# Performance work log

Hardware: AMD Instinct MI355X
Metric: run time of the kernel (lower is better)

Reference implementation:

```python
import jax, jax.numpy as jnp
import numpy as np

B, S, K, N, G = 4, 2048, 4096, 11008, 128  # batch, seq, in_features, out_features, groupsize


def setup_inputs() -> dict:
    key = jax.random.key(0)
    k1, k2, k3, k4 = jax.random.split(key, 4)
    x = jax.random.normal(k1, (B, S, K), dtype=jnp.float32)
    # unpacked int4 codes in [0, 16)
    weight_q = jax.random.randint(k2, (N, K), 0, 16, dtype=jnp.int32)
    # groupwise scales (positive, small) and zeros, packed as [K//G, N, 2]
    scales = jax.random.uniform(k3, (K // G, N), dtype=jnp.float32) * 0.02 + 1e-3
    zeros = jax.random.normal(k4, (K // G, N), dtype=jnp.float32) * 0.1
    scales_and_zeros = jnp.stack([scales, zeros], axis=-1)  # [K//G, N, 2]
    return {"x": x, "weight_q": weight_q, "scales_and_zeros": scales_and_zeros}


def reference(x, weight_q, scales_and_zeros):
    # Dequantize groupwise: w[n,k] = (q[n,k] - 8) * scale[k//G, n] + zero[k//G, n]
    scales = scales_and_zeros[..., 0].T  # [N, K//G]
    zeros = scales_and_zeros[..., 1].T   # [N, K//G]
    q = weight_q.astype(x.dtype).reshape(N, K // G, G)  # [N, K//G, G]
    w = (q - 8.0) * scales[:, :, None] + zeros[:, :, None]  # fused dequant
    w = w.reshape(N, K)
    # y[b,s,n] = sum_k x[b,s,k] * w[n,k]
    return jnp.einsum("bsk,nk->bsn", x, w)
```

## Files before the change

kernel.cpp:

```cpp
#include <hip/hip_runtime.h>
#include <stdint.h>


typedef __attribute__((ext_vector_type(8))) short short8;
typedef __attribute__((ext_vector_type(4))) float float4v;
typedef __attribute__((ext_vector_type(4))) int int4v;
typedef __attribute__((ext_vector_type(2))) float float2v;
typedef __attribute__((ext_vector_type(4))) unsigned short ushort4v;

static constexpr int M_ = 8192;
static constexpr int K_ = 4096;
static constexpr int N_ = 11008;
static constexpr int NKT = K_ / 64;

__device__ __forceinline__ unsigned short f2bf(float f) {
    union { float f; uint32_t u; } v;
    v.f = f;
    uint32_t u = v.u;
    u += 0x7fffu + ((u >> 16) & 1u);
    return (unsigned short)(u >> 16);
}

__device__ __forceinline__ void gload16(const void* g, void* l) {
    __builtin_amdgcn_global_load_lds(
        (const __attribute__((address_space(1))) uint32_t*)g,
        (__attribute__((address_space(3))) uint32_t*)l, 16, 0, 0);
}

__global__ __launch_bounds__(256) void cvt_x_kernel(const float* __restrict__ X,
                                                    unsigned short* __restrict__ Xb) {
    const int i = blockIdx.x * 256 + threadIdx.x;
    const float4v a = ((const float4v*)X)[2 * (size_t)i];
    const float4v b = ((const float4v*)X)[2 * (size_t)i + 1];
    short8 o;
    #pragma unroll
    for (int j = 0; j < 4; ++j) o[j] = (short)f2bf(a[j]);
    #pragma unroll
    for (int j = 0; j < 4; ++j) o[4 + j] = (short)f2bf(b[j]);
    ((short8*)Xb)[(size_t)i] = o;
}

__global__ __launch_bounds__(256) void deq_w_kernel(const int* __restrict__ Q,
                                                    const float* __restrict__ SZ,
                                                    unsigned short* __restrict__ Wb) {
    const int i = blockIdx.x * 256 + threadIdx.x;
    const int n = i >> 9;
    const int c = i & 511;
    const int k0 = c * 8;
    const int g = k0 >> 7;
    const float2v sz = *(const float2v*)(SZ + ((size_t)g * N_ + n) * 2);
    const float s = sz[0], z = sz[1];
    const int4v q0 = *(const int4v*)(Q + (size_t)n * K_ + k0);
    const int4v q1 = *(const int4v*)(Q + (size_t)n * K_ + k0 + 4);
    short8 o;
    #pragma unroll
    for (int j = 0; j < 4; ++j) o[j] = (short)f2bf((float)(q0[j] - 8) * s + z);
    #pragma unroll
    for (int j = 0; j < 4; ++j) o[4 + j] = (short)f2bf((float)(q1[j] - 8) * s + z);
    ((short8*)Wb)[(size_t)i] = o;
}


template <int BUF, int MH>
__device__ __forceinline__ void read_a(const char* ldsB, short8 (&a)[4][2],
                                       int aK0, int aK1) {
    constexpr int base = BUF * 32768 + MH * 16384;
    #pragma unroll
    for (int i = 0; i < 4; ++i) {
        a[i][0] = *(const short8*)(ldsB + base + i * 2048 + aK0);
        a[i][1] = *(const short8*)(ldsB + base + i * 2048 + aK1);
    }
}

template <int BUF, int NH>
__device__ __forceinline__ void read_b(const char* ldsB, short8 (&b)[2][2],
                                       int bK0, int bK1) {
    constexpr int base = BUF * 32768 + NH * 16384;
    #pragma unroll
    for (int j = 0; j < 2; ++j) {
        b[j][0] = *(const short8*)(ldsB + base + j * 2048 + bK0);
        b[j][1] = *(const short8*)(ldsB + base + j * 2048 + bK1);
    }
}

template <int MH, int NH>
__device__ __forceinline__ void phase_mma(short8 (&a)[4][2], short8 (&b)[2][2],
                                          float4v (&acc)[8][4]) {
    __builtin_amdgcn_s_setprio(1);
    #pragma unroll
    for (int i = 0; i < 4; ++i)
        #pragma unroll
        for (int j = 0; j < 2; ++j) {
            acc[MH * 4 + i][NH * 2 + j] = __builtin_amdgcn_mfma_f32_16x16x32_bf16(
                a[i][0], b[j][0], acc[MH * 4 + i][NH * 2 + j], 0, 0, 0);
            acc[MH * 4 + i][NH * 2 + j] = __builtin_amdgcn_mfma_f32_16x16x32_bf16(
                a[i][1], b[j][1], acc[MH * 4 + i][NH * 2 + j], 0, 0, 0);
        }
    __builtin_amdgcn_s_setprio(0);
}

#define SBAR() __builtin_amdgcn_sched_barrier(0)
#define VMW(n) asm volatile("s_waitcnt vmcnt(" #n ")" ::: "memory")
#define LGKM(n) asm volatile("s_waitcnt lgkmcnt(" #n ")" ::: "memory")
#define BARRIER() __builtin_amdgcn_s_barrier()

__global__ __launch_bounds__(512, 2) void gemm_bf16_8ph(
    const unsigned short* __restrict__ Agl,
    const unsigned short* __restrict__ Bgl,
    float* __restrict__ C) {
    __shared__ alignas(16) unsigned short lds[65536];

    const int tid = threadIdx.x;
    const int lane = tid & 63;
    const int wid = tid >> 6;
    const int wr = wid >> 2;
    const int wc = wid & 3;

    const int bid = blockIdx.x;
    const int wg = (bid & 7) * 172 + (bid >> 3);
    const int mt = wg / 43;
    const int nt = wg % 43;
    const int row0 = mt * 256;
    const int col0 = nt * 256;

    const int r8 = lane >> 3;
    const int kc = ((lane & 7) ^ r8) * 8;

    const int l15 = lane & 15;
    const int k0o = ((lane >> 4) * 16) ^ ((l15 & 7) << 4);
    const int k1o = k0o ^ 64;
    const int aK0 = (wr * 64 + l15) * 128 + k0o;
    const int aK1 = (wr * 64 + l15) * 128 + k1o;
    const int bK0 = 65536 + (wc * 32 + l15) * 128 + k0o;
    const int bK1 = 65536 + (wc * 32 + l15) * 128 + k1o;
    const char* ldsB = (const char*)lds;
    unsigned short* ldsU = lds;
    const char* AglB = (const char*)Agl;
    const char* BglB = (const char*)Bgl;

    uint32_t sA[2][2], sB[2][2];
    #pragma unroll
    for (int h = 0; h < 2; ++h)
        #pragma unroll
        for (int i = 0; i < 2; ++i) {
            sA[h][i] = (uint32_t)(row0 + h * 128 + (wid * 2 + i) * 8 + r8) * (K_ * 2)
                       + (uint32_t)kc * 2;
            sB[h][i] = (uint32_t)(col0 + h * 128 + (wid * 2 + i) * 8 + r8) * (K_ * 2)
                       + (uint32_t)kc * 2;
        }

    auto gA = [&](uint32_t& off, int b, int h, int i) {
        gload16(AglB + off, ldsU + b * 16384 + (h * 128 + (wid * 2 + i) * 8) * 64);
        off += 128;
    };
    auto gB = [&](uint32_t& off, int b, int h, int i) {
        gload16(BglB + off, ldsU + 32768 + b * 16384 + (h * 128 + (wid * 2 + i) * 8) * 64);
        off += 128;
    };

    float4v acc[8][4] = {};

    gA(sA[0][0], 0, 0, 0); gA(sA[0][1], 0, 0, 1);
    gB(sB[0][0], 0, 0, 0); gB(sB[0][1], 0, 0, 1);
    gB(sB[1][0], 0, 1, 0); gB(sB[1][1], 0, 1, 1);
    gA(sA[1][0], 0, 1, 0); gA(sA[1][1], 0, 1, 1);
    VMW(4);
    BARRIER(); SBAR();

#define KTILE(BUF, DN, W1, W2, W3, DOEND)                                   \
    {                                                                       \
        short8 a0[4][2], a1[4][2], b0[2][2], b1[2][2];                      \
                                   \
        read_a<BUF, 0>(ldsB, a0, aK0, aK1);                                 \
        read_b<BUF, 0>(ldsB, b0, bK0, bK1);                                 \
        if (DN) { gA(sA[0][0], (BUF) ^ 1, 0, 0); gA(sA[0][1], (BUF) ^ 1, 0, 1); } \
        LGKM(8);                                                            \
        BARRIER(); SBAR();                                                  \
        LGKM(0); SBAR();                                                    \
        phase_mma<0, 0>(a0, b0, acc);                                       \
        VMW(W1);                                                            \
        BARRIER(); SBAR();                                                  \
                                       \
        read_b<BUF, 1>(ldsB, b1, bK0, bK1);                                 \
        if (DN) { gB(sB[0][0], (BUF) ^ 1, 0, 0); gB(sB[0][1], (BUF) ^ 1, 0, 1); } \
        BARRIER(); SBAR();                                                  \
        LGKM(0); SBAR();                                                    \
        phase_mma<0, 1>(a0, b1, acc);                                       \
        VMW(W2);                                                            \
        BARRIER(); SBAR();                                                  \
                                       \
        read_a<BUF, 1>(ldsB, a1, aK0, aK1);                                 \
        if (DN) { gB(sB[1][0], (BUF) ^ 1, 1, 0); gB(sB[1][1], (BUF) ^ 1, 1, 1); } \
        BARRIER(); SBAR();                                                  \
        LGKM(0); SBAR();                                                    \
        phase_mma<1, 0>(a1, b0, acc);                                       \
        BARRIER(); SBAR();                                                  \
                                          \
        if (DN) { gA(sA[1][0], (BUF) ^ 1, 1, 0); gA(sA[1][1], (BUF) ^ 1, 1, 1); } \
        phase_mma<1, 1>(a1, b1, acc);                                       \
        if (DOEND) {                                                        \
            VMW(W3);                                                        \
            BARRIER(); SBAR();                                              \
        }                                                                   \
    }

    for (int t2 = 0; t2 < NKT - 2; t2 += 2) {
        KTILE(0, 1, 4, 4, 4, 1);
        KTILE(1, 1, 4, 4, 4, 1);
    }
    KTILE(0, 1, 4, 4, 4, 1);
    KTILE(1, 0, 2, 0, 0, 0);
#undef KTILE

    const int lrow = (lane >> 4) * 4;
    #pragma unroll
    for (int mf = 0; mf < 8; ++mf)
        #pragma unroll
        for (int nf = 0; nf < 4; ++nf)
            #pragma unroll
            for (int j = 0; j < 4; ++j) {
                const int r = row0 + (mf >> 2) * 128 + wr * 64 + (mf & 3) * 16 + lrow + j;
                const int c = col0 + (nf >> 1) * 128 + wc * 32 + (nf & 1) * 16 + l15;
                C[(size_t)r * N_ + c] = acc[mf][nf][j];
            }
}

static constexpr int LDSS = 40;

__global__ __launch_bounds__(256, 2) void w4_gemm_fused(
    const float* __restrict__ X, const int* __restrict__ Q,
    const float* __restrict__ SZ, float* __restrict__ C) {
    __shared__ alignas(16) unsigned short As[128 * LDSS];
    __shared__ alignas(16) unsigned short Ws[128 * LDSS];
    const int tid = threadIdx.x;
    const int lane = tid & 63;
    const int wid = tid >> 6;
    const int wrr = wid >> 1;
    const int wcc = wid & 1;
    const int row0 = blockIdx.x * 128;
    const int col0 = blockIdx.y * 128;
    float4v acc[4][4] = {};
    float4v a_reg[4];
    int4v q_reg[4];
    float2v sz_reg[4];

    auto load_tile = [&](int kb) {
        const int g = kb >> 7;
        #pragma unroll
        for (int i = 0; i < 4; ++i) {
            const int idx = tid + 256 * i;
            const int r = idx >> 3;
            const int v = idx & 7;
            a_reg[i] = *(const float4v*)(X + (size_t)(row0 + r) * K_ + kb + v * 4);
            q_reg[i] = *(const int4v*)(Q + (size_t)(col0 + r) * K_ + kb + v * 4);
            sz_reg[i] = *(const float2v*)(SZ + ((size_t)g * N_ + (col0 + r)) * 2);
        }
    };
    auto write_tile = [&]() {
        #pragma unroll
        for (int i = 0; i < 4; ++i) {
            const int idx = tid + 256 * i;
            const int r = idx >> 3;
            const int v = idx & 7;
            ushort4v ab, wb;
            #pragma unroll
            for (int j = 0; j < 4; ++j) ab[j] = f2bf(a_reg[i][j]);
            const float s = sz_reg[i][0];
            const float z = sz_reg[i][1];
            #pragma unroll
            for (int j = 0; j < 4; ++j) wb[j] = f2bf((float)(q_reg[i][j] - 8) * s + z);
            *(ushort4v*)(&As[r * LDSS + v * 4]) = ab;
            *(ushort4v*)(&Ws[r * LDSS + v * 4]) = wb;
        }
    };
    auto compute = [&]() {
        const int lr = lane & 15;
        const int lg = lane >> 4;
        short8 af[4], bf[4];
        #pragma unroll
        for (int mf = 0; mf < 4; ++mf)
            af[mf] = *(const short8*)(&As[(wrr * 64 + mf * 16 + lr) * LDSS + lg * 8]);
        #pragma unroll
        for (int nf = 0; nf < 4; ++nf)
            bf[nf] = *(const short8*)(&Ws[(wcc * 64 + nf * 16 + lr) * LDSS + lg * 8]);
        #pragma unroll
        for (int mf = 0; mf < 4; ++mf)
            #pragma unroll
            for (int nf = 0; nf < 4; ++nf)
                acc[mf][nf] = __builtin_amdgcn_mfma_f32_16x16x32_bf16(
                    af[mf], bf[nf], acc[mf][nf], 0, 0, 0);
    };

    load_tile(0);
    for (int kb = 0; kb < K_; kb += 32) {
        __syncthreads();
        write_tile();
        __syncthreads();
        if (kb + 32 < K_) load_tile(kb + 32);
        compute();
    }
    const int lr = lane & 15;
    const int lg = lane >> 4;
    #pragma unroll
    for (int mf = 0; mf < 4; ++mf)
        #pragma unroll
        for (int nf = 0; nf < 4; ++nf)
            #pragma unroll
            for (int j = 0; j < 4; ++j) {
                const int r = row0 + wrr * 64 + mf * 16 + lg * 4 + j;
                const int c = col0 + wcc * 64 + nf * 16 + lr;
                C[(size_t)r * N_ + c] = acc[mf][nf][j];
            }
}

extern "C" void kernel_launch(void* const* d_in, const int* in_sizes, int n_in,
                              void* d_out, int out_size, void* d_ws, size_t ws_size,
                              hipStream_t stream) {
    const float* X  = (const float*)d_in[0];
    const int*   Q  = (const int*)d_in[1];
    const float* SZ = (const float*)d_in[2];
    float* C = (float*)d_out;

    const size_t xb_bytes = (size_t)M_ * K_ * 2;
    const size_t wb_bytes = (size_t)N_ * K_ * 2;
    if (ws_size >= xb_bytes + wb_bytes) {
        unsigned short* Xb = (unsigned short*)d_ws;
        unsigned short* Wb = (unsigned short*)((char*)d_ws + xb_bytes);
        cvt_x_kernel<<<(M_ * (K_ / 8)) / 256, 256, 0, stream>>>(X, Xb);
        deq_w_kernel<<<(N_ * (K_ / 8)) / 256, 256, 0, stream>>>(Q, SZ, Wb);
        gemm_bf16_8ph<<<dim3(1376), dim3(512), 0, stream>>>(Xb, Wb, C);
    } else {
        dim3 grid(M_ / 128, N_ / 128);
        w4_gemm_fused<<<grid, dim3(256), 0, stream>>>(X, Q, SZ, C);
    }
}
```

Before: 750.4 us.

## Switch GEMM inner loop to 32x32x16 bf16 MFMA with new LDS fragment layout

Replaces the 16x16x32 MFMA tiles with 32x32x16 MFMA instructions, restructuring accumulators into 4x2 float16 vectors and recomputing swizzled LDS read offsets for four k-slices per fragment. The larger MFMA shape raises the arithmetic per LDS read and per instruction issue, aiming to cut LDS traffic and instruction overhead in the bf16 GEMM. The epilogue is rewritten for the 32x32 output register layout. The new swizzle and layout mapping risk bank conflicts or correctness errors if the offsets do not match the global-to-LDS write pattern.

```diff
diff --git a/kernel.cpp b/kernel.cpp
--- a/kernel.cpp
+++ b/kernel.cpp
@@ -3,6 +3,7 @@
 
 
 typedef __attribute__((ext_vector_type(8))) short short8;
+typedef __attribute__((ext_vector_type(16))) float float16v;
 typedef __attribute__((ext_vector_type(4))) float float4v;
 typedef __attribute__((ext_vector_type(4))) int int4v;
 typedef __attribute__((ext_vector_type(2))) float float2v;
@@ -61,44 +62,6 @@
 }
 
 
-template <int BUF, int MH>
-__device__ __forceinline__ void read_a(const char* ldsB, short8 (&a)[4][2],
-                                       int aK0, int aK1) {
-    constexpr int base = BUF * 32768 + MH * 16384;
-    #pragma unroll
-    for (int i = 0; i < 4; ++i) {
-        a[i][0] = *(const short8*)(ldsB + base + i * 2048 + aK0);
-        a[i][1] = *(const short8*)(ldsB + base + i * 2048 + aK1);
-    }
-}
-
-template <int BUF, int NH>
-__device__ __forceinline__ void read_b(const char* ldsB, short8 (&b)[2][2],
-                                       int bK0, int bK1) {
-    constexpr int base = BUF * 32768 + NH * 16384;
-    #pragma unroll
-    for (int j = 0; j < 2; ++j) {
-        b[j][0] = *(const short8*)(ldsB + base + j * 2048 + bK0);
-        b[j][1] = *(const short8*)(ldsB + base + j * 2048 + bK1);
-    }
-}
-
-template <int MH, int NH>
-__device__ __forceinline__ void phase_mma(short8 (&a)[4][2], short8 (&b)[2][2],
-                                          float4v (&acc)[8][4]) {
-    __builtin_amdgcn_s_setprio(1);
-    #pragma unroll
-    for (int i = 0; i < 4; ++i)
-        #pragma unroll
-        for (int j = 0; j < 2; ++j) {
-            acc[MH * 4 + i][NH * 2 + j] = __builtin_amdgcn_mfma_f32_16x16x32_bf16(
-                a[i][0], b[j][0], acc[MH * 4 + i][NH * 2 + j], 0, 0, 0);
-            acc[MH * 4 + i][NH * 2 + j] = __builtin_amdgcn_mfma_f32_16x16x32_bf16(
-                a[i][1], b[j][1], acc[MH * 4 + i][NH * 2 + j], 0, 0, 0);
-        }
-    __builtin_amdgcn_s_setprio(0);
-}
-
 #define SBAR() __builtin_amdgcn_sched_barrier(0)
 #define VMW(n) asm volatile("s_waitcnt vmcnt(" #n ")" ::: "memory")
 #define LGKM(n) asm volatile("s_waitcnt lgkmcnt(" #n ")" ::: "memory")
@@ -126,13 +89,15 @@
     const int r8 = lane >> 3;
     const int kc = ((lane & 7) ^ r8) * 8;
 
-    const int l15 = lane & 15;
-    const int k0o = ((lane >> 4) * 16) ^ ((l15 & 7) << 4);
-    const int k1o = k0o ^ 64;
-    const int aK0 = (wr * 64 + l15) * 128 + k0o;
-    const int aK1 = (wr * 64 + l15) * 128 + k1o;
-    const int bK0 = 65536 + (wc * 32 + l15) * 128 + k0o;
-    const int bK1 = 65536 + (wc * 32 + l15) * 128 + k1o;
+    const int l31 = lane & 31;
+    const int g5 = lane >> 5;
+    int aO[4], bO[4];
+    #pragma unroll
+    for (int ks = 0; ks < 4; ++ks) {
+        const int ko = (((ks * 2 + g5) ^ (lane & 7)) << 4);
+        aO[ks] = wr * 8192 + l31 * 128 + ko;
+        bO[ks] = 65536 + wc * 4096 + l31 * 128 + ko;
+    }
     const char* ldsB = (const char*)lds;
     unsigned short* ldsU = lds;
     const char* AglB = (const char*)Agl;
@@ -158,7 +123,17 @@
         off += 128;
     };
 
-    float4v acc[8][4] = {};
+    float16v acc[4][2] = {};
+
+#define RDA(DST, CB, MH, MI, KS) \
+    DST[MI][KS] = *(const short8*)(ldsB + (CB) + (MH)*16384 + (MI)*4096 + aO[KS]);
+#define RDB(DST, CB, NH, KS) \
+    DST[KS] = *(const short8*)(ldsB + (CB) + (NH)*16384 + bO[KS]);
+#define MMA4(MF, NF, A, MI, B)                                              \
+    acc[MF][NF] = __builtin_amdgcn_mfma_f32_32x32x16_bf16(A[MI][0], B[0], acc[MF][NF], 0, 0, 0); \
+    acc[MF][NF] = __builtin_amdgcn_mfma_f32_32x32x16_bf16(A[MI][1], B[1], acc[MF][NF], 0, 0, 0); \
+    acc[MF][NF] = __builtin_amdgcn_mfma_f32_32x32x16_bf16(A[MI][2], B[2], acc[MF][NF], 0, 0, 0); \
+    acc[MF][NF] = __builtin_amdgcn_mfma_f32_32x32x16_bf16(A[MI][3], B[3], acc[MF][NF], 0, 0, 0);
 
     gA(sA[0][0], 0, 0, 0); gA(sA[0][1], 0, 0, 1);
     gB(sB[0][0], 0, 0, 0); gB(sB[0][1], 0, 0, 1);
@@ -169,35 +144,50 @@
 
 #define KTILE(BUF, DN, W1, W2, W3, DOEND)                                   \
     {                                                                       \
-        short8 a0[4][2], a1[4][2], b0[2][2], b1[2][2];                      \
+        constexpr int CB = (BUF) * 32768;                                   \
+        short8 a01[2][4], a23[2][4], b0[4], b1[4];                          \
                                    \
-        read_a<BUF, 0>(ldsB, a0, aK0, aK1);                                 \
-        read_b<BUF, 0>(ldsB, b0, bK0, bK1);                                 \
+        RDA(a01, CB, 0, 0, 0) RDA(a01, CB, 0, 0, 1)                         \
+        RDA(a01, CB, 0, 0, 2) RDA(a01, CB, 0, 0, 3)                         \
+        RDA(a01, CB, 0, 1, 0) RDA(a01, CB, 0, 1, 1)                         \
+        RDA(a01, CB, 0, 1, 2) RDA(a01, CB, 0, 1, 3)                         \
+        RDB(b0, CB, 0, 0) RDB(b0, CB, 0, 1) RDB(b0, CB, 0, 2) RDB(b0, CB, 0, 3) \
         if (DN) { gA(sA[0][0], (BUF) ^ 1, 0, 0); gA(sA[0][1], (BUF) ^ 1, 0, 1); } \
         LGKM(8);                                                            \
         BARRIER(); SBAR();                                                  \
         LGKM(0); SBAR();                                                    \
-        phase_mma<0, 0>(a0, b0, acc);                                       \
+        __builtin_amdgcn_s_setprio(1);                                      \
+        MMA4(0, 0, a01, 0, b0) MMA4(1, 0, a01, 1, b0)                       \
+        __builtin_amdgcn_s_setprio(0);                                      \
         VMW(W1);                                                            \
         BARRIER(); SBAR();                                                  \
-                                       \
-        read_b<BUF, 1>(ldsB, b1, bK0, bK1);                                 \
+                                         \
+        RDB(b1, CB, 1, 0) RDB(b1, CB, 1, 1) RDB(b1, CB, 1, 2) RDB(b1, CB, 1, 3) \
         if (DN) { gB(sB[0][0], (BUF) ^ 1, 0, 0); gB(sB[0][1], (BUF) ^ 1, 0, 1); } \
         BARRIER(); SBAR();                                                  \
         LGKM(0); SBAR();                                                    \
-        phase_mma<0, 1>(a0, b1, acc);                                       \
+        __builtin_amdgcn_s_setprio(1);                                      \
+        MMA4(0, 1, a01, 0, b1) MMA4(1, 1, a01, 1, b1)                       \
+        __builtin_amdgcn_s_setprio(0);                                      \
         VMW(W2);                                                            \
         BARRIER(); SBAR();                                                  \
-                                       \
-        read_a<BUF, 1>(ldsB, a1, aK0, aK1);                                 \
+                                         \
+        RDA(a23, CB, 1, 0, 0) RDA(a23, CB, 1, 0, 1)                         \
+        RDA(a23, CB, 1, 0, 2) RDA(a23, CB, 1, 0, 3)                         \
+        RDA(a23, CB, 1, 1, 0) RDA(a23, CB, 1, 1, 1)                         \
+        RDA(a23, CB, 1, 1, 2) RDA(a23, CB, 1, 1, 3)                         \
         if (DN) { gB(sB[1][0], (BUF) ^ 1, 1, 0); gB(sB[1][1], (BUF) ^ 1, 1, 1); } \
         BARRIER(); SBAR();                                                  \
         LGKM(0); SBAR();                                                    \
-        phase_mma<1, 0>(a1, b0, acc);                                       \
+        __builtin_amdgcn_s_setprio(1);                                      \
+        MMA4(2, 0, a23, 0, b0) MMA4(3, 0, a23, 1, b0)                       \
+        __builtin_amdgcn_s_setprio(0);                                      \
         BARRIER(); SBAR();                                                  \
                                           \
         if (DN) { gA(sA[1][0], (BUF) ^ 1, 1, 0); gA(sA[1][1], (BUF) ^ 1, 1, 1); } \
-        phase_mma<1, 1>(a1, b1, acc);                                       \
+        __builtin_amdgcn_s_setprio(1);                                      \
+        MMA4(2, 1, a23, 0, b1) MMA4(3, 1, a23, 1, b1)                       \
+        __builtin_amdgcn_s_setprio(0);                                      \
         if (DOEND) {                                                        \
             VMW(W3);                                                        \
             BARRIER(); SBAR();                                              \
@@ -211,18 +201,22 @@
     KTILE(0, 1, 4, 4, 4, 1);
     KTILE(1, 0, 2, 0, 0, 0);
 #undef KTILE
-
-    const int lrow = (lane >> 4) * 4;
-    #pragma unroll
-    for (int mf = 0; mf < 8; ++mf)
-        #pragma unroll
-        for (int nf = 0; nf < 4; ++nf)
-            #pragma unroll
-            for (int j = 0; j < 4; ++j) {
-                const int r = row0 + (mf >> 2) * 128 + wr * 64 + (mf & 3) * 16 + lrow + j;
-                const int c = col0 + (nf >> 1) * 128 + wc * 32 + (nf & 1) * 16 + l15;
-                C[(size_t)r * N_ + c] = acc[mf][nf][j];
+#undef RDA
+#undef RDB
+#undef MMA4
+
+    #pragma unroll
+    for (int mf = 0; mf < 4; ++mf)
+        #pragma unroll
+        for (int nf = 0; nf < 2; ++nf) {
+            const int rbase = row0 + (mf >> 1) * 128 + wr * 64 + (mf & 1) * 32 + 4 * g5;
+            const int c = col0 + nf * 128 + wc * 32 + l31;
+            #pragma unroll
+            for (int reg = 0; reg < 16; ++reg) {
+                const int r = rbase + (reg & 3) + 8 * (reg >> 2);
+                C[(size_t)r * N_ + c] = acc[mf][nf][reg];
             }
+        }
 }
 
 static constexpr int LDSS = 40;
```

Measured after the change: 847.0 us. +12.9%, slower.
